# Kernel tuning notes

Measured on AMD Instinct MI355X. Metric: run time of the kernel, lower is better.

Reference implementation:

```python
import jax, jax.numpy as jnp
import numpy as np


def setup_inputs() -> dict:
    key = jax.random.key(0)
    ks = jax.random.split(key, 8)
    B, C, N = 32, 1024, 512  # N must equal in_dim for the Linear path
    s = 0.02
    return {
        "x": jax.random.normal(ks[0], (B, C, N), dtype=jnp.float32),
        "Wq": jax.random.normal(ks[1], (N, N), dtype=jnp.float32) * s,
        "bq": jax.random.normal(ks[2], (N,), dtype=jnp.float32) * s,
        "Wk": jax.random.normal(ks[3], (N, N), dtype=jnp.float32) * s,
        "bk": jax.random.normal(ks[4], (N,), dtype=jnp.float32) * s,
        "Wv": jax.random.normal(ks[5], (N, N), dtype=jnp.float32) * s,
        "bv": jax.random.normal(ks[6], (N,), dtype=jnp.float32) * s,
        "beta": jax.random.normal(ks[7], (1,), dtype=jnp.float32),
    }


def reference(x, Wq, bq, Wk, bk, Wv, bv, beta):
    # torch Linear applies to the last axis: y = x @ W.T + b
    q = jnp.einsum('bcn,mn->bcm', x, Wq) + bq  # (B, C, N)
    k = jnp.einsum('bcn,mn->bcm', x, Wk) + bk  # (B, C, N)
    v = jnp.einsum('bcn,mn->bcm', x, Wv) + bv  # (B, C, N)
    # energy = bmm(q, k^T) over channel axis -> (B, C, C); NO 1/sqrt(d) scaling
    energy = jnp.einsum('bcn,bdn->bcd', q, k)
    attention = jax.nn.softmax(energy, axis=-1)
    out_x = jnp.einsum('bcd,bdn->bcn', attention, v)  # (B, C, N)
    out = beta * out_x + v  # beta-scaled residual onto the VALUE projection
    return out
```

## Files before the change

kernel.cpp:

```cpp
#include <hip/hip_runtime.h>
#include <hip/hip_bf16.h>

typedef short s8v __attribute__((ext_vector_type(8)));
typedef float f4v __attribute__((ext_vector_type(4)));

#define MFMA_BF16(a, b, c) __builtin_amdgcn_mfma_f32_16x16x32_bf16((a), (b), (c), 0, 0, 0)

#define GLDS16(g, l) __builtin_amdgcn_global_load_lds( \
    (const __attribute__((address_space(1))) void*)(g), \
    (__attribute__((address_space(3))) void*)(l), 16, 0, 0)

__device__ __forceinline__ short f2bf(float f) {
  __hip_bfloat16 h = __float2bfloat16(f);
  return *reinterpret_cast<short*>(&h);
}
__device__ __forceinline__ float bf2f(short s) {
  __hip_bfloat16 h;
  *reinterpret_cast<short*>(&h) = s;
  return __bfloat162float(h);
}

__global__ __launch_bounds__(256) void cvt_kernel(const float* __restrict__ in,
                                                  short* __restrict__ out, int n8) {
  int i = blockIdx.x * 256 + threadIdx.x;
  if (i >= n8) return;
  const float* p = in + (size_t)i * 8;
  float4 a = *(const float4*)p;
  float4 b = *(const float4*)(p + 4);
  s8v o;
  o[0] = f2bf(a.x); o[1] = f2bf(a.y); o[2] = f2bf(a.z); o[3] = f2bf(a.w);
  o[4] = f2bf(b.x); o[5] = f2bf(b.y); o[6] = f2bf(b.z); o[7] = f2bf(b.w);
  *(s8v*)(out + (size_t)i * 8) = o;
}

template<int KSTEPS, int ASTR, int BSTR>
__device__ __forceinline__ void mm_core(const short* __restrict__ Abase,
                                        const short* __restrict__ Bbase,
                                        short* As0, short* Bs0,
                                        short* As1, short* Bs1,
                                        f4v (&acc)[4][4]) {
  const int t = threadIdx.x;
  const int lane = t & 63, w = t >> 6;
  const int lr = lane & 15, lg = lane >> 4;
  const int wr = (w >> 1) * 64, wc = (w & 1) * 64;
  const int srcc = ((lane & 7) * 16) ^ ((lane >> 3) << 4);
  const int rstage = w * 32 + (lane >> 3);

  auto stage = [&](short* As, short* Bs, int kt) {
    #pragma unroll
    for (int j = 0; j < 4; ++j)
      GLDS16((const char*)(Abase + (size_t)(rstage + j * 8) * ASTR) + kt * 128 + srcc,
             (char*)As + (w * 32 + j * 8) * 128);
    #pragma unroll
    for (int j = 0; j < 4; ++j)
      GLDS16((const char*)(Bbase + (size_t)(rstage + j * 8) * BSTR) + kt * 128 + srcc,
             (char*)Bs + (w * 32 + j * 8) * 128);
  };

  stage(As0, Bs0, 0);
  if (KSTEPS > 1) stage(As1, Bs1, 1);
  short* Asc = As0; short* Bsc = Bs0;
  short* Asn = As1; short* Bsn = Bs1;

  for (int kt = 0; kt < KSTEPS; ++kt) {
    if (kt + 1 < KSTEPS) asm volatile("s_waitcnt vmcnt(8)" ::: "memory");
    else                 asm volatile("s_waitcnt vmcnt(0)" ::: "memory");
    __builtin_amdgcn_s_barrier();
    #pragma unroll
    for (int kk = 0; kk < 2; ++kk) {
      s8v af[4], bfr[4];
      #pragma unroll
      for (int mf = 0; mf < 4; ++mf)
        af[mf] = *(const s8v*)((const char*)Asc + (wr + mf * 16 + lr) * 128 +
                               ((kk * 64 + lg * 16) ^ ((lr & 7) << 4)));
      #pragma unroll
      for (int nf = 0; nf < 4; ++nf)
        bfr[nf] = *(const s8v*)((const char*)Bsc + (wc + nf * 16 + lr) * 128 +
                                ((kk * 64 + lg * 16) ^ ((lr & 7) << 4)));
      if (kk == 1) {
        asm volatile("s_waitcnt lgkmcnt(0)" ::: "memory");
        __builtin_amdgcn_s_barrier();
        if (kt + 2 < KSTEPS) stage(Asc, Bsc, kt + 2);
      }
      __builtin_amdgcn_s_setprio(1);
      #pragma unroll
      for (int mf = 0; mf < 4; ++mf)
        #pragma unroll
        for (int nf = 0; nf < 4; ++nf)
          acc[mf][nf] = MFMA_BF16(af[mf], bfr[nf], acc[mf][nf]);
      __builtin_amdgcn_s_setprio(0);
    }
    short* ta = Asc; Asc = Asn; Asn = ta;
    short* tb = Bsc; Bsc = Bsn; Bsn = tb;
  }
}

__global__ __launch_bounds__(256) void proj_kernel(
    const short* __restrict__ xb, const short* __restrict__ wb,
    const float* __restrict__ bq, const float* __restrict__ bk, const float* __restrict__ bv,
    short* __restrict__ qo, short* __restrict__ ko, short* __restrict__ vo) {
  const int bx = blockIdx.x;
  const int L = (bx & 7) * 384 + (bx >> 3);
  const int cb = L & 3, rb = (L >> 2) & 255, mat = L >> 10;
  const int R0 = rb * 128, C0 = cb * 128;
  const float* bias = (mat == 0) ? bq : (mat == 1) ? bk : bv;
  short* out = (mat == 0) ? qo : (mat == 1) ? ko : vo;

  __shared__ short As0[8192], Bs0[8192], As1[8192], Bs1[8192];
  f4v acc[4][4];
  #pragma unroll
  for (int i = 0; i < 4; i++)
    #pragma unroll
    for (int j = 0; j < 4; j++) acc[i][j] = (f4v){0.f, 0.f, 0.f, 0.f};

  mm_core<8, 512, 512>(xb + (size_t)R0 * 512,
                       wb + (size_t)mat * 512 * 512 + (size_t)C0 * 512,
                       As0, Bs0, As1, Bs1, acc);

  const int lane = threadIdx.x & 63, w = threadIdx.x >> 6;
  const int lr = lane & 15, lg = lane >> 4;
  const int wr = (w >> 1) * 64, wc = (w & 1) * 64;
  #pragma unroll
  for (int nf = 0; nf < 4; ++nf) {
    int col = C0 + wc + nf * 16 + lr;
    float bb = bias[col];
    #pragma unroll
    for (int mf = 0; mf < 4; ++mf)
      #pragma unroll
      for (int i = 0; i < 4; i++) {
        int row = R0 + wr + mf * 16 + lg * 4 + i;
        out[(size_t)row * 512 + col] = f2bf(acc[mf][nf][i] + bb);
      }
  }
}

__global__ __launch_bounds__(256) void transpose_kernel(const short* __restrict__ v,
                                                        short* __restrict__ vt) {
  const int nb = blockIdx.x;
  const int cbk = blockIdx.y;
  const int b = blockIdx.z;
  __shared__ short tile[64 * 72];
  const int t = threadIdx.x;
  const int r = t >> 2, qd = t & 3;
  const short* src = v + (size_t)(b * 1024 + cbk * 64 + r) * 512 + nb * 64 + qd * 16;
  s8v v0 = *(const s8v*)src;
  s8v v1 = *(const s8v*)(src + 8);
  *(s8v*)&tile[r * 72 + qd * 16] = v0;
  *(s8v*)&tile[r * 72 + qd * 16 + 8] = v1;
  __syncthreads();
  s8v o0, o1;
  #pragma unroll
  for (int j = 0; j < 8; j++) o0[j] = tile[(qd * 16 + j) * 72 + r];
  #pragma unroll
  for (int j = 0; j < 8; j++) o1[j] = tile[(qd * 16 + 8 + j) * 72 + r];
  short* dst = vt + (size_t)(b * 512 + nb * 64 + r) * 1024 + cbk * 64 + qd * 16;
  *(s8v*)dst = o0;
  *(s8v*)(dst + 8) = o1;
}

__global__ __launch_bounds__(256) void qk_kernel(const short* __restrict__ qb,
                                                 const short* __restrict__ kb,
                                                 short* __restrict__ eb) {
  const int bx = blockIdx.x;
  const int L = (bx & 7) * 256 + (bx >> 3);
  const int rb = L & 7, cb = (L >> 3) & 7, b = L >> 6;
  const int R0 = rb * 128, C0 = cb * 128;

  __shared__ short As0[8192], Bs0[8192], As1[8192], Bs1[8192];
  f4v acc[4][4];
  #pragma unroll
  for (int i = 0; i < 4; i++)
    #pragma unroll
    for (int j = 0; j < 4; j++) acc[i][j] = (f4v){0.f, 0.f, 0.f, 0.f};

  mm_core<8, 512, 512>(qb + (size_t)(b * 1024 + R0) * 512,
                       kb + (size_t)(b * 1024 + C0) * 512,
                       As0, Bs0, As1, Bs1, acc);

  const int lane = threadIdx.x & 63, w = threadIdx.x >> 6;
  const int lr = lane & 15, lg = lane >> 4;
  const int wr = (w >> 1) * 64, wc = (w & 1) * 64;
  #pragma unroll
  for (int nf = 0; nf < 4; ++nf) {
    int col = C0 + wc + nf * 16 + lr;
    #pragma unroll
    for (int mf = 0; mf < 4; ++mf)
      #pragma unroll
      for (int i = 0; i < 4; i++) {
        int row = R0 + wr + mf * 16 + lg * 4 + i;
        eb[(size_t)(b * 1024 + row) * 1024 + col] = f2bf(acc[mf][nf][i]);
      }
  }
}

__global__ __launch_bounds__(256) void softmax_kernel(short* __restrict__ eb) {
  const int row = blockIdx.x * 4 + (threadIdx.x >> 6);
  const int lane = threadIdx.x & 63;
  short* p = eb + (size_t)row * 1024 + lane * 16;
  s8v a = *(const s8v*)p;
  s8v bvv = *(const s8v*)(p + 8);
  float v[16];
  #pragma unroll
  for (int j = 0; j < 8; j++) { v[j] = bf2f(a[j]); v[8 + j] = bf2f(bvv[j]); }
  float m = v[0];
  #pragma unroll
  for (int j = 1; j < 16; j++) m = fmaxf(m, v[j]);
  #pragma unroll
  for (int s = 1; s <= 32; s <<= 1) m = fmaxf(m, __shfl_xor(m, s));
  float l = 0.f;
  #pragma unroll
  for (int j = 0; j < 16; j++) { v[j] = __expf(v[j] - m); l += v[j]; }
  #pragma unroll
  for (int s = 1; s <= 32; s <<= 1) l += __shfl_xor(l, s);
  const float inv = 1.0f / l;
  s8v o0, o1;
  #pragma unroll
  for (int j = 0; j < 8; j++) { o0[j] = f2bf(v[j] * inv); o1[j] = f2bf(v[8 + j] * inv); }
  *(s8v*)p = o0;
  *(s8v*)(p + 8) = o1;
}

__global__ __launch_bounds__(256) void pv_kernel(const short* __restrict__ eb,
                                                 const short* __restrict__ vt,
                                                 const short* __restrict__ vb,
                                                 const float* __restrict__ beta_p,
                                                 float* __restrict__ outp) {
  const int bx = blockIdx.x;
  const int L = (bx & 7) * 128 + (bx >> 3);
  const int cb = L & 3, rb = (L >> 2) & 7, b = L >> 5;
  const int R0 = rb * 128, C0 = cb * 128;

  __shared__ short As0[8192], Bs0[8192], As1[8192], Bs1[8192];
  f4v acc[4][4];
  #pragma unroll
  for (int i = 0; i < 4; i++)
    #pragma unroll
    for (int j = 0; j < 4; j++) acc[i][j] = (f4v){0.f, 0.f, 0.f, 0.f};

  mm_core<16, 1024, 1024>(eb + (size_t)(b * 1024 + R0) * 1024,
                          vt + (size_t)(b * 512 + C0) * 1024,
                          As0, Bs0, As1, Bs1, acc);

  const float beta = beta_p[0];
  const int lane = threadIdx.x & 63, w = threadIdx.x >> 6;
  const int lr = lane & 15, lg = lane >> 4;
  const int wr = (w >> 1) * 64, wc = (w & 1) * 64;
  #pragma unroll
  for (int nf = 0; nf < 4; ++nf) {
    int col = C0 + wc + nf * 16 + lr;
    #pragma unroll
    for (int mf = 0; mf < 4; ++mf)
      #pragma unroll
      for (int i = 0; i < 4; i++) {
        int row = R0 + wr + mf * 16 + lg * 4 + i;
        float val = beta * acc[mf][nf][i] +
                    bf2f(vb[(size_t)(b * 1024 + row) * 512 + col]);
        outp[(size_t)(b * 1024 + row) * 512 + col] = val;
      }
  }
}

extern "C" void kernel_launch(void* const* d_in, const int* in_sizes, int n_in,
                              void* d_out, int out_size, void* d_ws, size_t ws_size,
                              hipStream_t stream) {
  (void)in_sizes; (void)n_in; (void)out_size; (void)ws_size;
  const float* x = (const float*)d_in[0];
  const float* Wq = (const float*)d_in[1];
  const float* bq = (const float*)d_in[2];
  const float* Wk = (const float*)d_in[3];
  const float* bk = (const float*)d_in[4];
  const float* Wv = (const float*)d_in[5];
  const float* bv = (const float*)d_in[6];
  const float* beta = (const float*)d_in[7];
  float* out = (float*)d_out;

  char* ws = (char*)d_ws;
  short* xb = (short*)(ws);
  short* wb = (short*)(ws + 33554432);
  short* qb = (short*)(ws + 35127296);
  short* kb = (short*)(ws + 68681728);
  short* vb = (short*)(ws + 102236160);
  short* eb = (short*)(ws + 135790592);
  short* vt = xb;

  cvt_kernel<<<8192, 256, 0, stream>>>(x, xb, 2097152);
  cvt_kernel<<<128, 256, 0, stream>>>(Wq, wb, 32768);
  cvt_kernel<<<128, 256, 0, stream>>>(Wk, wb + 262144, 32768);
  cvt_kernel<<<128, 256, 0, stream>>>(Wv, wb + 524288, 32768);
  proj_kernel<<<3072, 256, 0, stream>>>(xb, wb, bq, bk, bv, qb, kb, vb);
  transpose_kernel<<<dim3(8, 16, 32), 256, 0, stream>>>(vb, vt);
  qk_kernel<<<2048, 256, 0, stream>>>(qb, kb, eb);
  softmax_kernel<<<8192, 256, 0, stream>>>(eb);
  pv_kernel<<<1024, 256, 0, stream>>>(eb, vt, vb, beta, out);
}
```

Measured before the change: 220.2 us.

## Fuse V transpose into projection epilogue and merge weight conversions

The projection kernel now also writes a transposed copy of V, staged through shared memory in its epilogue, so the separate transpose kernel can be skipped when the workspace is large enough for a dedicated vt buffer. The three weight-conversion launches are merged into a single kernel. The aim is to drop one full read and write pass over V plus two launches, at the cost of extra LDS stores, a barrier and strided global writes in the V blocks of the projection kernel. The fused path depends on the workspace size, so if the workspace is too small the original transpose path still runs.

```diff
diff --git a/kernel.cpp b/kernel.cpp
--- a/kernel.cpp
+++ b/kernel.cpp
@@ -31,6 +31,22 @@
   o[0] = f2bf(a.x); o[1] = f2bf(a.y); o[2] = f2bf(a.z); o[3] = f2bf(a.w);
   o[4] = f2bf(b.x); o[5] = f2bf(b.y); o[6] = f2bf(b.z); o[7] = f2bf(b.w);
   *(s8v*)(out + (size_t)i * 8) = o;
+}
+
+__global__ __launch_bounds__(256) void cvt_w_kernel(const float* __restrict__ Wq,
+                                                    const float* __restrict__ Wk,
+                                                    const float* __restrict__ Wv,
+                                                    short* __restrict__ out) {
+  int i = blockIdx.x * 256 + threadIdx.x;
+  int mat = i >> 15, idx = i & 32767;
+  const float* src = (mat == 0) ? Wq : (mat == 1) ? Wk : Wv;
+  const float* p = src + (size_t)idx * 8;
+  float4 a = *(const float4*)p;
+  float4 b = *(const float4*)(p + 4);
+  s8v o;
+  o[0] = f2bf(a.x); o[1] = f2bf(a.y); o[2] = f2bf(a.z); o[3] = f2bf(a.w);
+  o[4] = f2bf(b.x); o[5] = f2bf(b.y); o[6] = f2bf(b.z); o[7] = f2bf(b.w);
+  *(s8v*)(out + (size_t)mat * 262144 + (size_t)idx * 8) = o;
 }
 
 template<int KSTEPS, int ASTR, int BSTR>
@@ -98,7 +114,8 @@
 __global__ __launch_bounds__(256) void proj_kernel(
     const short* __restrict__ xb, const short* __restrict__ wb,
     const float* __restrict__ bq, const float* __restrict__ bk, const float* __restrict__ bv,
-    short* __restrict__ qo, short* __restrict__ ko, short* __restrict__ vo) {
+    short* __restrict__ qo, short* __restrict__ ko, short* __restrict__ vo,
+    short* __restrict__ vt, int fuse) {
   const int bx = blockIdx.x;
   const int L = (bx & 7) * 384 + (bx >> 3);
   const int cb = L & 3, rb = (L >> 2) & 255, mat = L >> 10;
@@ -106,7 +123,12 @@
   const float* bias = (mat == 0) ? bq : (mat == 1) ? bk : bv;
   short* out = (mat == 0) ? qo : (mat == 1) ? ko : vo;
 
-  __shared__ short As0[8192], Bs0[8192], As1[8192], Bs1[8192];
+  __shared__ short smem[32768];
+  short* As0 = smem;
+  short* Bs0 = smem + 8192;
+  short* As1 = smem + 16384;
+  short* Bs1 = smem + 24576;
+
   f4v acc[4][4];
   #pragma unroll
   for (int i = 0; i < 4; i++)
@@ -120,6 +142,8 @@
   const int lane = threadIdx.x & 63, w = threadIdx.x >> 6;
   const int lr = lane & 15, lg = lane >> 4;
   const int wr = (w >> 1) * 64, wc = (w & 1) * 64;
+  const bool dovt = (mat == 2) && (fuse != 0);
+  short* lds_t = smem;
   #pragma unroll
   for (int nf = 0; nf < 4; ++nf) {
     int col = C0 + wc + nf * 16 + lr;
@@ -128,9 +152,20 @@
     for (int mf = 0; mf < 4; ++mf)
       #pragma unroll
       for (int i = 0; i < 4; i++) {
-        int row = R0 + wr + mf * 16 + lg * 4 + i;
-        out[(size_t)row * 512 + col] = f2bf(acc[mf][nf][i] + bb);
+        int rloc = wr + mf * 16 + lg * 4 + i;
+        short bv16 = f2bf(acc[mf][nf][i] + bb);
+        out[(size_t)(R0 + rloc) * 512 + col] = bv16;
+        if (dovt) lds_t[(wc + nf * 16 + lr) * 136 + rloc] = bv16;
       }
+  }
+  if (dovt) {
+    __syncthreads();
+    const int b = R0 >> 10, c0 = R0 & 1023;
+    const int n_l = threadIdx.x >> 1, ch = (threadIdx.x & 1) * 64;
+    const short* srcp = lds_t + n_l * 136 + ch;
+    short* dstp = vt + ((size_t)(b * 512 + C0 + n_l)) * 1024 + c0 + ch;
+    #pragma unroll
+    for (int j = 0; j < 8; ++j) *(s8v*)(dstp + j * 8) = *(const s8v*)(srcp + j * 8);
   }
 }
 
@@ -263,7 +298,7 @@
 extern "C" void kernel_launch(void* const* d_in, const int* in_sizes, int n_in,
                               void* d_out, int out_size, void* d_ws, size_t ws_size,
                               hipStream_t stream) {
-  (void)in_sizes; (void)n_in; (void)out_size; (void)ws_size;
+  (void)in_sizes; (void)n_in; (void)out_size;
   const float* x = (const float*)d_in[0];
   const float* Wq = (const float*)d_in[1];
   const float* bq = (const float*)d_in[2];
@@ -281,14 +316,14 @@
   short* kb = (short*)(ws + 68681728);
   short* vb = (short*)(ws + 102236160);
   short* eb = (short*)(ws + 135790592);
-  short* vt = xb;
+
+  const int fuse = (ws_size >= 236453888ull) ? 1 : 0;
+  short* vt = fuse ? (short*)(ws + 202899456) : xb;
 
   cvt_kernel<<<8192, 256, 0, stream>>>(x, xb, 2097152);
-  cvt_kernel<<<128, 256, 0, stream>>>(Wq, wb, 32768);
-  cvt_kernel<<<128, 256, 0, stream>>>(Wk, wb + 262144, 32768);
-  cvt_kernel<<<128, 256, 0, stream>>>(Wv, wb + 524288, 32768);
-  proj_kernel<<<3072, 256, 0, stream>>>(xb, wb, bq, bk, bv, qb, kb, vb);
-  transpose_kernel<<<dim3(8, 16, 32), 256, 0, stream>>>(vb, vt);
+  cvt_w_kernel<<<384, 256, 0, stream>>>(Wq, Wk, Wv, wb);
+  proj_kernel<<<3072, 256, 0, stream>>>(xb, wb, bq, bk, bv, qb, kb, vb, vt, fuse);
+  if (!fuse) transpose_kernel<<<dim3(8, 16, 32), 256, 0, stream>>>(vb, vt);
   qk_kernel<<<2048, 256, 0, stream>>>(qb, kb, eb);
   softmax_kernel<<<8192, 256, 0, stream>>>(eb);
   pv_kernel<<<1024, 256, 0, stream>>>(eb, vt, vb, beta, out);
```

New measurement: 239.3 us. 1.09x slower.
